# Kernel tuning notes

Hardware: AMD Instinct MI355X
Metric: run time of the kernel (lower is better)

Reference implementation:

```python
import jax, jax.numpy as jnp
import numpy as np

BLOCK = 8
EMBED = 16
VOCAB = 29
B = 131072


def setup_inputs() -> dict:
    key = jax.random.key(0)
    ks = jax.random.split(key, 8)
    s = 0.05
    return {
        "idx": jax.random.randint(ks[0], (B, BLOCK), 0, VOCAB),
        "tok_table": jax.random.normal(ks[1], (VOCAB, EMBED), jnp.float32) * s,
        "pos_table": jax.random.normal(ks[2], (BLOCK, EMBED), jnp.float32) * s,
        "Wk": jax.random.normal(ks[3], (EMBED, EMBED), jnp.float32) * s,
        "Wq": jax.random.normal(ks[4], (EMBED, EMBED), jnp.float32) * s,
        "Wv": jax.random.normal(ks[5], (EMBED, EMBED), jnp.float32) * s,
        "lm_W": jax.random.normal(ks[6], (VOCAB, EMBED), jnp.float32) * s,
        "lm_b": jax.random.normal(ks[7], (VOCAB,), jnp.float32) * s,
    }


def reference(idx, tok_table, pos_table, Wk, Wq, Wv, lm_W, lm_b):
    T = idx.shape[1]
    # embed + positional add: [B, T, E]
    x = tok_table[idx] + pos_table[:T]
    # single-head causal self-attention (torch Linear: y = x @ W.T)
    k = jnp.einsum('bte,he->bth', x, Wk)
    q = jnp.einsum('bte,he->bth', x, Wq)
    v = jnp.einsum('bte,he->bth', x, Wv)
    scale = EMBED ** -0.5  # source scales by C**-0.5 with C = embed_size
    wei = jnp.einsum('bqh,bkh->bqk', q, k) * scale  # [B, T, T]
    causal = jnp.tril(jnp.ones((T, T), dtype=bool))
    wei = jnp.where(causal, wei, -jnp.inf)
    wei = jax.nn.softmax(wei, axis=-1)
    out = jnp.einsum('bqk,bkh->bqh', wei, v)  # [B, T, E]
    logits = jnp.einsum('bth,vh->btv', out, lm_W) + lm_b  # [B, T, VOCAB]
    return logits
```

## Files before the change

### kernel.cpp

```cpp
#include <hip/hip_runtime.h>
#include <hip/hip_bf16.h>
#include <stdint.h>

#define NVOC 29

#define OFF_LM 1372
#define OFF_B  (1372 + 29*233)
#define TAB_TOTAL 8158

__device__ float g_tab[TAB_TOTAL];

__device__ __forceinline__ float b2f(__hip_bfloat16 v) { return __bfloat162float(v); }
__device__ __forceinline__ float ldin(const void* p, int i, bool isf32) {
    return isf32 ? ((const float*)p)[i] : b2f(((const __hip_bfloat16*)p)[i]);
}

__global__ void prep_kernel(const void* __restrict__ tok, const void* __restrict__ pos,
                            const void* __restrict__ Wk,  const void* __restrict__ Wq,
                            const void* __restrict__ Wv,  const void* __restrict__ lmW,
                            const void* __restrict__ lmb) {
    __shared__ float sTQ[29][17], sTK[29][17], sTV[29][17];
    __shared__ float sPQ[8][17],  sPK[8][17],  sPV[8][17];
    __shared__ float sLW[29][17];
    const int tid = threadIdx.x;

    const uint32_t* tw = (const uint32_t*)tok;
    int cnt = 0;
    #pragma unroll
    for (int wi = 0; wi < 32; ++wi) {
        uint32_t x = tw[wi];
        uint32_t e0 = (x >> 7) & 0xFF, e1 = (x >> 23) & 0xFF;
        cnt += (e0 >= 96 && e0 <= 132) ? 1 : 0;
        cnt += (e1 >= 96 && e1 <= 132) ? 1 : 0;
    }
    const bool isf32 = (cnt < 54);

    for (int i = tid; i < 29 * 16; i += 256) sLW[i >> 4][i & 15] = ldin(lmW, i, isf32);

    for (int i = tid; i < 111 * 16; i += 256) {
        const int h = i & 15, rt = i >> 4;
        const void* xp; int xo; const void* wp; float* dst;
        if (rt < 29)       { xp = tok; xo = rt * 16;         wp = Wq; dst = &sTQ[rt][h]; }
        else if (rt < 58)  { xp = tok; xo = (rt - 29) * 16;  wp = Wk; dst = &sTK[rt - 29][h]; }
        else if (rt < 87)  { xp = tok; xo = (rt - 58) * 16;  wp = Wv; dst = &sTV[rt - 58][h]; }
        else if (rt < 95)  { xp = pos; xo = (rt - 87) * 16;  wp = Wq; dst = &sPQ[rt - 87][h]; }
        else if (rt < 103) { xp = pos; xo = (rt - 95) * 16;  wp = Wk; dst = &sPK[rt - 95][h]; }
        else               { xp = pos; xo = (rt - 103) * 16; wp = Wv; dst = &sPV[rt - 103][h]; }
        float s = 0.f;
        #pragma unroll
        for (int e = 0; e < 16; ++e)
            s += ldin(xp, xo + e, isf32) * ldin(wp, h * 16 + e, isf32);
        *dst = s;
    }
    __syncthreads();

    const float f = 0.25f * 1.44269504088896340736f;

    for (int g = blockIdx.x * 256 + tid; g < TAB_TOTAL; g += gridDim.x * 256) {
        float val = 0.f;
        if (g < 841) {
            int a = g / 29, c = g % 29; float s = 0.f;
            #pragma unroll
            for (int h = 0; h < 16; ++h) s += sTQ[a][h] * sTK[c][h];
            val = f * s;
        } else if (g < 1073) {
            int o = g - 841, a = o >> 3, u = o & 7; float s = 0.f;
            #pragma unroll
            for (int h = 0; h < 16; ++h) s += sTQ[a][h] * sPK[u][h];
            val = f * s;
        } else if (g < 1305) {
            int o = g - 1073, t = o / 29, c = o % 29; float s = 0.f;
            #pragma unroll
            for (int h = 0; h < 16; ++h) s += sPQ[t][h] * sTK[c][h];
            val = f * s;
        } else if (g < 1369) {
            int o = g - 1305, t = o >> 3, u = o & 7; float s = 0.f;
            #pragma unroll
            for (int h = 0; h < 16; ++h) s += sPQ[t][h] * sPK[u][h];
            val = f * s;
        } else if (g >= OFF_LM && g < OFF_B) {
            int o = g - OFF_LM, a = o / 233, r = o % 233;
            if (r < 232) {
                int u = r / 29, v = r % 29; float s = 0.f;
                #pragma unroll
                for (int h = 0; h < 16; ++h) s += (sTV[a][h] + sPV[u][h]) * sLW[v][h];
                val = s;
            }
        } else if (g >= OFF_B) {
            int v = g - OFF_B;
            if (v < NVOC) val = ldin(lmb, v, isf32);
        }
        g_tab[g] = val;
    }
}

__global__ __launch_bounds__(512, 4)
void main_kernel(const int* __restrict__ idxg, float* __restrict__ out) {
    __shared__ __attribute__((aligned(16))) float s_mem[512 * NVOC];
    __shared__ int sIdx[512];

    const int tid = threadIdx.x;
    const int blk = blockIdx.x;

    for (int i = tid; i < TAB_TOTAL; i += 512) s_mem[i] = g_tab[i];
    sIdx[tid] = idxg[blk * 512 + tid];
    __syncthreads();

    const int t  = tid >> 6;
    const int lb = tid & 63;

    int iu[8];
    #pragma unroll
    for (int u = 0; u < 8; ++u) iu[u] = sIdx[lb * 8 + u];
    const int it = iu[t];

    float w[8];
    #pragma unroll
    for (int u = 0; u < 8; ++u) {
        float wu = s_mem[it * 29 + iu[u]]
                 + s_mem[841 + it * 8 + u]
                 + s_mem[1073 + t * 29 + iu[u]]
                 + s_mem[1305 + t * 8 + u];
        w[u] = (u <= t) ? wu : -1.0e30f;
    }
    float mx = w[0];
    #pragma unroll
    for (int u = 1; u < 8; ++u) mx = fmaxf(mx, w[u]);
    float ssum = 0.f;
    #pragma unroll
    for (int u = 0; u < 8; ++u) { float e = exp2f(w[u] - mx); w[u] = e; ssum += e; }
    const float inv = 1.0f / ssum;

    float acc[NVOC];
    #pragma unroll
    for (int v = 0; v < NVOC; ++v) acc[v] = 0.f;
    #pragma unroll
    for (int u = 0; u < 8; ++u) if (u <= t) {
        const float pu = w[u];
        const int base = OFF_LM + iu[u] * 233 + u * 29;
        #pragma unroll
        for (int v = 0; v < NVOC; ++v) acc[v] = fmaf(pu, s_mem[base + v], acc[v]);
    }
    #pragma unroll
    for (int v = 0; v < NVOC; ++v) acc[v] = fmaf(acc[v], inv, s_mem[OFF_B + v]);
    __syncthreads();

    const int orow = (lb * 8 + t) * NVOC;
    #pragma unroll
    for (int v = 0; v < NVOC; ++v) s_mem[orow + v] = acc[v];
    __syncthreads();

    const uint4* src = (const uint4*)s_mem;
    uint4* dst = (uint4*)(out + (size_t)blk * (512 * NVOC));
    for (int i = tid; i < 3712; i += 512) dst[i] = src[i];
}

extern "C" void kernel_launch(void* const* d_in, const int* in_sizes, int n_in,
                              void* d_out, int out_size, void* d_ws, size_t ws_size,
                              hipStream_t stream) {
    const int* idx = (const int*)d_in[0];
    const void* tok = d_in[1];
    const void* pos = d_in[2];
    const void* Wk  = d_in[3];
    const void* Wq  = d_in[4];
    const void* Wv  = d_in[5];
    const void* lmW = d_in[6];
    const void* lmb = d_in[7];
    float* out = (float*)d_out;

    const int B = in_sizes[0] / 8;
    const int nblk = B / 64;

    hipLaunchKernelGGL(prep_kernel, dim3(16), dim3(256), 0, stream,
                       tok, pos, Wk, Wq, Wv, lmW, lmb);
    hipLaunchKernelGGL(main_kernel, dim3(nblk), dim3(512), 0, stream,
                       idx, out);
}
```

Before: 183.4 us.

## Pad precomputed tables to 32-wide rows and vectorize main kernel LDS access

Re-lays out the precomputed score and logit tables with rows padded to 32 (or 65 float4) so the main kernel can read them with float4 LDS loads and shift/mask indexing instead of divisions. Index rows are loaded directly from global memory as int4, which removes the shared index staging. The output is now staged in two halves through a swizzled shared buffer sized to the table, which cuts LDS use and lets launch bounds request 6 blocks per CU. The cost is extra barriers and scalar, non-vector global stores with division-based index math in the write-out.

Measured after the change: 185.5 us. Within noise of the previous version (+1.1%).

```diff
diff --git a/kernel.cpp b/kernel.cpp
--- a/kernel.cpp
+++ b/kernel.cpp
@@ -3,12 +3,9 @@
 #include <stdint.h>
 
 #define NVOC 29
-
-#define OFF_LM 1372
-#define OFF_B  (1372 + 29*233)
-#define TAB_TOTAL 8158
-
-__device__ float g_tab[TAB_TOTAL];
+#define TABW 9056
+
+__device__ __attribute__((aligned(16))) float g_tab[TABW];
 
 __device__ __forceinline__ float b2f(__hip_bfloat16 v) { return __bfloat162float(v); }
 __device__ __forceinline__ float ldin(const void* p, int i, bool isf32) {
@@ -56,71 +53,79 @@
 
     const float f = 0.25f * 1.44269504088896340736f;
 
-    for (int g = blockIdx.x * 256 + tid; g < TAB_TOTAL; g += gridDim.x * 256) {
+    for (int g = blockIdx.x * 256 + tid; g < TABW; g += gridDim.x * 256) {
         float val = 0.f;
-        if (g < 841) {
-            int a = g / 29, c = g % 29; float s = 0.f;
-            #pragma unroll
-            for (int h = 0; h < 16; ++h) s += sTQ[a][h] * sTK[c][h];
-            val = f * s;
-        } else if (g < 1073) {
-            int o = g - 841, a = o >> 3, u = o & 7; float s = 0.f;
+        if (g < 928) {
+            int a = g >> 5, c = g & 31;
+            if (c < 29) { float s = 0.f;
+                #pragma unroll
+                for (int h = 0; h < 16; ++h) s += sTQ[a][h] * sTK[c][h];
+                val = f * s; }
+        } else if (g < 1160) {
+            int o = g - 928, a = o >> 3, u = o & 7; float s = 0.f;
             #pragma unroll
             for (int h = 0; h < 16; ++h) s += sTQ[a][h] * sPK[u][h];
             val = f * s;
-        } else if (g < 1305) {
-            int o = g - 1073, t = o / 29, c = o % 29; float s = 0.f;
-            #pragma unroll
-            for (int h = 0; h < 16; ++h) s += sPQ[t][h] * sTK[c][h];
-            val = f * s;
-        } else if (g < 1369) {
-            int o = g - 1305, t = o >> 3, u = o & 7; float s = 0.f;
+        } else if (g < 1416) {
+            int o = g - 1160, t = o >> 5, c = o & 31;
+            if (c < 29) { float s = 0.f;
+                #pragma unroll
+                for (int h = 0; h < 16; ++h) s += sPQ[t][h] * sTK[c][h];
+                val = f * s; }
+        } else if (g < 1480) {
+            int o = g - 1416, t = o >> 3, u = o & 7; float s = 0.f;
             #pragma unroll
             for (int h = 0; h < 16; ++h) s += sPQ[t][h] * sPK[u][h];
             val = f * s;
-        } else if (g >= OFF_LM && g < OFF_B) {
-            int o = g - OFF_LM, a = o / 233, r = o % 233;
-            if (r < 232) {
-                int u = r / 29, v = r % 29; float s = 0.f;
-                #pragma unroll
-                for (int h = 0; h < 16; ++h) s += (sTV[a][h] + sPV[u][h]) * sLW[v][h];
-                val = s;
+        } else if (g < 1512) {
+            int v = g - 1480;
+            if (v < NVOC) val = ldin(lmb, v, isf32);
+        } else if (g < 1512 + 29 * 260) {
+            int o = g - 1512, a = o / 260, r = o % 260;
+            if (r < 256) {
+                int u = r >> 5, v = r & 31;
+                if (v < NVOC) { float s = 0.f;
+                    #pragma unroll
+                    for (int h = 0; h < 16; ++h) s += (sTV[a][h] + sPV[u][h]) * sLW[v][h];
+                    val = s; }
             }
-        } else if (g >= OFF_B) {
-            int v = g - OFF_B;
-            if (v < NVOC) val = ldin(lmb, v, isf32);
         }
         g_tab[g] = val;
     }
 }
 
-__global__ __launch_bounds__(512, 4)
+__global__ __launch_bounds__(512, 6)
 void main_kernel(const int* __restrict__ idxg, float* __restrict__ out) {
-    __shared__ __attribute__((aligned(16))) float s_mem[512 * NVOC];
-    __shared__ int sIdx[512];
+    __shared__ __attribute__((aligned(16))) float s[TABW];
+    float4* s4 = (float4*)s;
 
     const int tid = threadIdx.x;
     const int blk = blockIdx.x;
-
-    for (int i = tid; i < TAB_TOTAL; i += 512) s_mem[i] = g_tab[i];
-    sIdx[tid] = idxg[blk * 512 + tid];
-    __syncthreads();
-
     const int t  = tid >> 6;
     const int lb = tid & 63;
 
-    int iu[8];
-    #pragma unroll
-    for (int u = 0; u < 8; ++u) iu[u] = sIdx[lb * 8 + u];
-    const int it = iu[t];
+    const int4* ig = (const int4*)(idxg + (size_t)blk * 512);
+    const int4 iA = ig[lb * 2], iB = ig[lb * 2 + 1];
+
+    const float4* gt4 = (const float4*)g_tab;
+    for (int i = tid; i < TABW / 4; i += 512) s4[i] = gt4[i];
+    __syncthreads();
+
+    const int iu[8] = { iA.x, iA.y, iA.z, iA.w, iB.x, iB.y, iB.z, iB.w };
+    const int it = (t == 0) ? iu[0] : (t == 1) ? iu[1] : (t == 2) ? iu[2] :
+                   (t == 3) ? iu[3] : (t == 4) ? iu[4] : (t == 5) ? iu[5] :
+                   (t == 6) ? iu[6] : iu[7];
+
+    const float4 qtpA = s4[232 + it * 2], qtpB = s4[233 + it * 2];
+    const float4 qppA = s4[354 + t * 2],  qppB = s4[355 + t * 2];
+    const float qtp[8] = { qtpA.x, qtpA.y, qtpA.z, qtpA.w, qtpB.x, qtpB.y, qtpB.z, qtpB.w };
+    const float qpp[8] = { qppA.x, qppA.y, qppA.z, qppA.w, qppB.x, qppB.y, qppB.z, qppB.w };
 
     float w[8];
     #pragma unroll
     for (int u = 0; u < 8; ++u) {
-        float wu = s_mem[it * 29 + iu[u]]
-                 + s_mem[841 + it * 8 + u]
-                 + s_mem[1073 + t * 29 + iu[u]]
-                 + s_mem[1305 + t * 8 + u];
+        float wu = s[it * 32 + iu[u]] + qtp[u]
+                 + s[1160 + t * 32 + iu[u]] + qpp[u];
         w[u] = (u <= t) ? wu : -1.0e30f;
     }
     float mx = w[0];
@@ -131,28 +136,52 @@
     for (int u = 0; u < 8; ++u) { float e = exp2f(w[u] - mx); w[u] = e; ssum += e; }
     const float inv = 1.0f / ssum;
 
-    float acc[NVOC];
-    #pragma unroll
-    for (int v = 0; v < NVOC; ++v) acc[v] = 0.f;
+    float4 acc[8];
+    #pragma unroll
+    for (int j = 0; j < 8; ++j) acc[j] = make_float4(0.f, 0.f, 0.f, 0.f);
     #pragma unroll
     for (int u = 0; u < 8; ++u) if (u <= t) {
         const float pu = w[u];
-        const int base = OFF_LM + iu[u] * 233 + u * 29;
+        const float4* r = s4 + 378 + iu[u] * 65 + u * 8;
         #pragma unroll
-        for (int v = 0; v < NVOC; ++v) acc[v] = fmaf(pu, s_mem[base + v], acc[v]);
-    }
-    #pragma unroll
-    for (int v = 0; v < NVOC; ++v) acc[v] = fmaf(acc[v], inv, s_mem[OFF_B + v]);
-    __syncthreads();
-
-    const int orow = (lb * 8 + t) * NVOC;
-    #pragma unroll
-    for (int v = 0; v < NVOC; ++v) s_mem[orow + v] = acc[v];
-    __syncthreads();
-
-    const uint4* src = (const uint4*)s_mem;
-    uint4* dst = (uint4*)(out + (size_t)blk * (512 * NVOC));
-    for (int i = tid; i < 3712; i += 512) dst[i] = src[i];
+        for (int j = 0; j < 8; ++j) {
+            float4 m = r[j];
+            acc[j].x = fmaf(pu, m.x, acc[j].x);
+            acc[j].y = fmaf(pu, m.y, acc[j].y);
+            acc[j].z = fmaf(pu, m.z, acc[j].z);
+            acc[j].w = fmaf(pu, m.w, acc[j].w);
+        }
+    }
+    #pragma unroll
+    for (int j = 0; j < 8; ++j) {
+        float4 b = s4[370 + j];
+        acc[j].x = fmaf(acc[j].x, inv, b.x);
+        acc[j].y = fmaf(acc[j].y, inv, b.y);
+        acc[j].z = fmaf(acc[j].z, inv, b.z);
+        acc[j].w = fmaf(acc[j].w, inv, b.w);
+    }
+
+    #pragma unroll
+    for (int h = 0; h < 2; ++h) {
+        __syncthreads();
+        if ((t >> 2) == h) {
+            const int rbase = (lb * 4 + (t & 3)) * 32;
+            #pragma unroll
+            for (int j = 0; j < 8; ++j) {
+                s[rbase + ((4 * j + 0 + lb) & 31)] = acc[j].x;
+                if (4 * j + 1 < NVOC) s[rbase + ((4 * j + 1 + lb) & 31)] = acc[j].y;
+                if (4 * j + 2 < NVOC) s[rbase + ((4 * j + 2 + lb) & 31)] = acc[j].z;
+                if (4 * j + 3 < NVOC) s[rbase + ((4 * j + 3 + lb) & 31)] = acc[j].w;
+            }
+        }
+        __syncthreads();
+        float* ob = out + (size_t)blk * (512 * NVOC) + h * 116;
+        for (int i = tid; i < 256 * NVOC; i += 512) {
+            int lbg = i / 116; int rr = i - lbg * 116;
+            int ttg = rr / 29; int vg = rr - ttg * 29;
+            ob[lbg * 232 + ttg * 29 + vg] = s[(lbg * 4 + ttg) * 32 + ((vg + lbg) & 31)];
+        }
+    }
 }
 
 extern "C" void kernel_launch(void* const* d_in, const int* in_sizes, int n_in,
```
